# Kernel tuning notes

Hardware: AMD Instinct MI355X
Metric: run time of the kernel (lower is better)

## Reference

```python
import jax, jax.numpy as jnp
import numpy as np

B, S, D, H = 4, 1024, 1024, 16
HD = D // H  # per-head dim = 64
NEG = -10000000000.0


def setup_inputs() -> dict:
    key = jax.random.key(0)
    ks = jax.random.split(key, 12)
    q = jax.random.normal(ks[0], (B, S, D), jnp.float32)
    k = jax.random.normal(ks[1], (B, S, D), jnp.float32)
    v = jax.random.normal(ks[2], (B, S, D), jnp.float32)
    mask = jax.random.randint(ks[3], (B, S, S), 0, 2).astype(jnp.int32)
    sc = 1.0 / np.sqrt(D)
    Wq = jax.random.normal(ks[4], (H, D, HD), jnp.float32) * sc
    bq = jnp.zeros((H, HD), jnp.float32)
    Wk = jax.random.normal(ks[5], (H, D, HD), jnp.float32) * sc
    bk = jnp.zeros((H, HD), jnp.float32)
    Wv = jax.random.normal(ks[6], (H, D, HD), jnp.float32) * sc
    bv = jnp.zeros((H, HD), jnp.float32)
    Wo = jax.random.normal(ks[7], (D, D), jnp.float32) * sc
    bo = jnp.zeros((D,), jnp.float32)
    return {"query": q, "key": k, "value": v, "attention_mask": mask,
            "Wq": Wq, "bq": bq, "Wk": Wk, "bk": bk, "Wv": Wv, "bv": bv,
            "Wo": Wo, "bo": bo}


def reference(query, key, value, attention_mask, Wq, bq, Wk, bk, Wv, bv, Wo, bo):
    # batched per-head projections: [B,S,D] x [H,D,E] -> [B,H,S,E]
    q = jnp.einsum('bsd,hde->bhse', query, Wq) + bq[None, :, None, :]
    k = jnp.einsum('bsd,hde->bhse', key, Wk) + bk[None, :, None, :]
    v = jnp.einsum('bsd,hde->bhse', value, Wv) + bv[None, :, None, :]
    # NOTE: scale uses key_dim (model_size = full D), faithful to source
    score = jnp.einsum('bhse,bhte->bhst', q, k) / jnp.sqrt(jnp.float32(D))
    m = attention_mask.astype(jnp.float32)[:, None, :, :]  # [B,1,S,S]
    score = score + (1.0 - m) * NEG
    attn = jax.nn.softmax(score, axis=-1) * m  # double masking
    heads = jnp.einsum('bhst,bhte->bhse', attn, v)  # [B,H,S,E]
    # concat heads along feature dim (head order preserved)
    heads = heads.transpose(0, 2, 1, 3).reshape(B, S, D)
    return heads @ Wo + bo
```

## Files before the change

kernel.cpp:

```cpp
#include <hip/hip_runtime.h>

#define B_ 4
#define S_ 1024
#define D_ 1024
#define H_ 16
#define E_ 64
#define BS_ (B_*S_)
#define BHSE_ (B_*H_*S_*E_)

typedef __attribute__((ext_vector_type(8))) short bf16x8;
typedef __attribute__((ext_vector_type(4))) float f32x4;
typedef __attribute__((ext_vector_type(4))) unsigned int u32x4;

__device__ __forceinline__ unsigned short f2bf(float f) {
    unsigned int x = __float_as_uint(f);
    x = (x + 0x7FFFu + ((x >> 16) & 1u)) >> 16;
    return (unsigned short)x;
}
__device__ __forceinline__ float bf2f(unsigned short u) {
    return __uint_as_float(((unsigned int)u) << 16);
}
__device__ __forceinline__ float ldin(const void* p, size_t i, int isb) {
    return isb ? bf2f(((const unsigned short*)p)[i]) : ((const float*)p)[i];
}

__device__ __forceinline__ unsigned int cvtpk(float lo, float hi) {
    unsigned int r;
    asm("v_cvt_pk_bf16_f32 %0, %1, %2" : "=v"(r) : "v"(lo), "v"(hi));
    return r;
}
__device__ __forceinline__ unsigned int bperm(int srclane4, unsigned int v) {
    return (unsigned int)__builtin_amdgcn_ds_bpermute(srclane4, (int)v);
}
__device__ __forceinline__ bf16x8 u4bf(u32x4 w) {
    union { u32x4 u; bf16x8 h; } c; c.u = w; return c.h;
}

#if __has_builtin(__builtin_amdgcn_exp2f)
#define EXP2(x) __builtin_amdgcn_exp2f(x)
#else
#define EXP2(x) __expf((x) * 0.6931471805599453f)
#endif

__device__ __forceinline__ void gl2lds16(const void* g, void* l) {
    __builtin_amdgcn_global_load_lds(
        (const __attribute__((address_space(1))) void*)g,
        (__attribute__((address_space(3))) void*)l, 16, 0, 0);
}

__device__ __forceinline__ int detect_isb(const unsigned int* q) {
    unsigned int wv = q[threadIdx.x & 63];
    unsigned int lo = wv & 0xFFFFu;
    unsigned int e = (lo >> 7) & 0xFFu;
    int ok = (lo == 0u) || (e >= 100u && e <= 145u);
    return __popcll(__ballot(ok)) >= 48;
}

__global__ __launch_bounds__(256) void preproc(
        const void* q_, const void* k_, const void* v_, const int* mask,
        const void* Wq, const void* Wk, const void* Wv, const void* Wo,
        const void* bq_, const void* bk_, const void* bv_, const void* bo_,
        unsigned short* WT, float* biases, unsigned long long* packT,
        unsigned short* Aconv) {
    __shared__ unsigned short Tt[64][72];
    const int isb = detect_isb((const unsigned int*)q_);
    const int blk = blockIdx.x, t = threadIdx.x;

    if (blk < 1024) {
        const int c0 = blk & 15, r0 = ((blk >> 4) & 15) * 64, z = blk >> 8;
        const void* src = (z == 0) ? Wq : (z == 1) ? Wk : (z == 2) ? Wv : Wo;
        {
            int dl = t >> 2, qc = t & 3;
            size_t base;
            if (z < 3) base = (size_t)c0 * 65536 + (size_t)(r0 + dl) * 64 + qc * 16;
            else       base = (size_t)(r0 + dl) * 1024 + (size_t)c0 * 64 + qc * 16;
            if (isb) {
                const unsigned short* s = (const unsigned short*)src + base;
                bf16x8 a0 = *(const bf16x8*)s, a1 = *(const bf16x8*)(s + 8);
#pragma unroll
                for (int j = 0; j < 8; j++) {
                    Tt[qc * 16 + j][dl] = (unsigned short)a0[j];
                    Tt[qc * 16 + 8 + j][dl] = (unsigned short)a1[j];
                }
            } else {
                const float* s = (const float*)src + base;
#pragma unroll
                for (int j = 0; j < 16; j++) Tt[qc * 16 + j][dl] = f2bf(s[j]);
            }
        }
        __syncthreads();
        {
            int el = t >> 2, qc = t & 3;
            size_t dst = (size_t)z * D_ * D_ + (size_t)(c0 * 64 + el) * D_ + r0 + qc * 16;
            *(bf16x8*)&WT[dst]     = *(const bf16x8*)&Tt[el][qc * 16];
            *(bf16x8*)&WT[dst + 8] = *(const bf16x8*)&Tt[el][qc * 16 + 8];
        }
        if (z == 3 && ((blk >> 4) & 15) == 0 && c0 < 4) {
            const void* bs = (c0 == 0) ? bq_ : (c0 == 1) ? bk_
                           : (c0 == 2) ? bv_ : bo_;
#pragma unroll
            for (int j = 0; j < 4; j++) {
                int i = t * 4 + j;
                biases[c0 * 1024 + i] = ldin(bs, i, isb);
            }
        }
    } else if (blk < 5120) {
        int unit = (blk - 1024) * 4 + (t >> 6);
        int lane = t & 63;
        int b = unit >> 12, rem = unit & 4095, s0 = (rem >> 4) * 4, kt = rem & 15;
        const int* mb = mask + ((size_t)b * 1024 + s0) * 1024 + kt * 64 + lane;
        unsigned long long bits[4];
#pragma unroll
        for (int j = 0; j < 4; j++) bits[j] = __ballot(mb[j * 1024] != 0);
        if (lane < 4) {
            unsigned long long bb = (lane == 0) ? bits[0] : (lane == 1) ? bits[1]
                                  : (lane == 2) ? bits[2] : bits[3];
            packT[((size_t)b * 16 + kt) * 1024 + s0 + lane] = bb;
        }
    } else {
        if (isb) return;
        int blk2 = blk - 5120;
        const int z = blk2 >> 11;
        const float* s = (z == 0) ? (const float*)q_ : (z == 1) ? (const float*)k_
                                                                : (const float*)v_;
        const size_t i = ((size_t)(blk2 & 2047) * 256 + t) * 8;
        f32x4 a0 = *(const f32x4*)(s + i);
        f32x4 a1 = *(const f32x4*)(s + i + 4);
        bf16x8 o;
#pragma unroll
        for (int j = 0; j < 4; j++) {
            o[j]     = (short)f2bf(a0[j]);
            o[4 + j] = (short)f2bf(a1[j]);
        }
        *(bf16x8*)&Aconv[(size_t)z * ((size_t)BS_ * D_) + i] = o;
    }
}

template<int BM, int BN, int MODE, int MINW>
__global__ __launch_bounds__(256, MINW) void gemm_k(
        const void* A0, const void* A1, const void* A2, const unsigned short* Aconv,
        const unsigned short* BtB, const float* biasB, void* dstB,
        const unsigned int* qdet) {
    constexpr int TOT16 = (BM + BN) * 32;
    constexpr int CALLS = TOT16 / 512;
    constexpr int CPW = CALLS / 4;
    constexpr int MT = BM / 32;
    constexpr int NT = BN / 32;
    __shared__ unsigned short buf[2][TOT16];

    const int fl = detect_isb(qdet);
    const int t = threadIdx.x, lane = t & 63, w = t >> 6;
    const int lm = lane & 15, q4 = lane >> 4;
    const int wm = w >> 1, wn = w & 1;
    const int lr = lane >> 2;
    const int ls = lane & 3;
    const int lg = ls ^ ((lr >> 1) & 3);

    const unsigned short* Abf;
    const unsigned short* Bt;
    const float* bias;
    int z = 0, m0, n0, phase;
    if (MODE == 0) {
        int bid = blockIdx.x + gridDim.x * (blockIdx.y + gridDim.y * blockIdx.z);
        int xcd = bid & 7, idx = bid >> 3;
        z = idx >> 5;
        int r = idx & 31;
        int mt = (xcd << 2) + (r & 3);
        int nt = r >> 2;
        m0 = mt * BM; n0 = nt * BN;
        phase = (nt * 13 + z * 5) & 31;
        const void* Ain = (z == 0) ? A0 : (z == 1 ? A1 : A2);
        Abf = fl ? (const unsigned short*)Ain
                 : Aconv + (size_t)z * ((size_t)BS_ * D_);
        Bt = BtB + (size_t)z * D_ * D_;
        bias = biasB + z * 1024;
    } else {
        Abf = (const unsigned short*)A0;
        Bt = BtB; bias = biasB;
        m0 = blockIdx.x * BM; n0 = blockIdx.y * BN;
        phase = (blockIdx.x * 7 + blockIdx.y * 13) & 31;
    }

    auto stage = [&](int kk, int bi) {
#pragma unroll
        for (int i = 0; i < CPW; ++i) {
            int c = w * CPW + i;
            int row = c * 16 + lr;
            const unsigned short* g;
            if (row < BM)
                g = Abf + (size_t)(m0 + row) * D_ + kk + lg * 8;
            else
                g = Bt + (size_t)(n0 + row - BM) * D_ + kk + lg * 8;
            gl2lds16(g, &buf[bi][c * 512]);
        }
    };

    f32x4 acc[MT][NT];
#pragma unroll
    for (int i = 0; i < MT; i++)
#pragma unroll
        for (int j = 0; j < NT; j++) acc[i][j] = (f32x4){0.f, 0.f, 0.f, 0.f};

    stage((phase & 31) * 32, 0);
    for (int it = 0; it < D_ / 32; ++it) {
        const int bi = it & 1;
        __syncthreads();
        if (it < D_ / 32 - 1) stage(((it + 1 + phase) & 31) * 32, bi ^ 1);

        const unsigned short* As = buf[bi];
        const unsigned short* Bs = buf[bi] + BM * 32;
        bf16x8 af[MT], bv[NT];
#pragma unroll
        for (int mt = 0; mt < MT; mt++) {
            int row = wm * (BM / 2) + mt * 16 + lm;
            af[mt] = *(const bf16x8*)&As[row * 32 + (q4 ^ ((row >> 1) & 3)) * 8];
        }
#pragma unroll
        for (int nt = 0; nt < NT; nt++) {
            int row = wn * (BN / 2) + nt * 16 + lm;
            bv[nt] = *(const bf16x8*)&Bs[row * 32 + (q4 ^ ((row >> 1) & 3)) * 8];
        }
#pragma unroll
        for (int mt = 0; mt < MT; mt++)
#pragma unroll
            for (int nt = 0; nt < NT; nt++)
                acc[mt][nt] = __builtin_amdgcn_mfma_f32_16x16x32_bf16(
                    af[mt], bv[nt], acc[mt][nt], 0, 0, 0);
    }

#pragma unroll
    for (int mt = 0; mt < MT; mt++)
#pragma unroll
        for (int nt = 0; nt < NT; nt++) {
            int N = n0 + wn * (BN / 2) + nt * 16 + lm;
            int Mb = m0 + wm * (BM / 2) + mt * 16 + q4 * 4;
            if (MODE == 0 && z == 2) {
                int bb = Mb >> 10, sb = Mb & 1023, hh = N >> 6, e = N & 63;
                unsigned long long hv = 0;
#pragma unroll
                for (int r = 0; r < 4; r++)
                    hv |= (unsigned long long)f2bf(acc[mt][nt][r] + bias[N]) << (16 * r);
                unsigned short* d16 = (unsigned short*)dstB + (size_t)2 * BHSE_;
                *(unsigned long long*)&d16[(((size_t)(bb * H_ + hh) * E_ + e) << 10) + sb] = hv;
            } else {
#pragma unroll
                for (int r = 0; r < 4; r++) {
                    int M = Mb + r;
                    float v = acc[mt][nt][r] + bias[N];
                    if (MODE == 0) {
                        int bb = M >> 10, s = M & 1023, hh = N >> 6, e = N & 63;
                        unsigned short* d16 = (unsigned short*)dstB + (size_t)z * BHSE_;
                        d16[((size_t)(bb * H_ + hh) * S_ + s) * E_ + e] = f2bf(v);
                    } else {
                        size_t idx = (size_t)M * D_ + N;
                        if (fl) ((unsigned short*)dstB)[idx] = f2bf(v);
                        else    ((float*)dstB)[idx] = v;
                    }
                }
            }
        }
}

__global__ __launch_bounds__(256, 5) void attn64(
        const unsigned short* Qp, const unsigned short* Kp, const unsigned short* VpT,
        const unsigned long long* packT, unsigned short* heads) {
    __shared__ unsigned short KT[2][4096];
    __shared__ unsigned short VT[2][4096];

    const int qt = blockIdx.x, h = blockIdx.y, b = blockIdx.z;
    const int t = threadIdx.x, w = t >> 6, lane = t & 63, lm = lane & 15, q4 = lane >> 4;
    const size_t bh = ((size_t)b * H_ + h) * S_ * E_;
    const unsigned short* Qb = Qp + bh;
    const unsigned short* Kb = Kp + bh;
    const unsigned short* Vb = VpT + bh;
    const int q0 = qt * 64 + w * 16;

    const int l3 = lane >> 3, l7 = lane & 7;
    const int kLaneOff = l3 * 64 + (l7 ^ l3) * 8;
    const int vLaneOff = l3 * 1024 + (l7 ^ l3) * 8;

    const int sw = lm & 7;
    const int c0 = (q4 ^ sw) * 8, c1 = ((q4 ^ 4) ^ sw) * 8;

    const int srcA4 = ((lane & 15) | ((lane & 16) << 1)) << 2;
    const int srcB4 = srcA4 + 64;
    const bool selHi = (lane & 32) != 0;

    bf16x8 bq0 = *(const bf16x8*)&Qb[(size_t)(q0 + lm) * E_ + q4 * 8];
    bf16x8 bq1 = *(const bf16x8*)&Qb[(size_t)(q0 + lm) * E_ + 32 + q4 * 8];

    f32x4 oacc[4];
#pragma unroll
    for (int i = 0; i < 4; i++) oacc[i] = (f32x4){0.f, 0.f, 0.f, 0.f};
    float mrun = -3.0e38f, lrun = 0.f;
    const float scale2 = 0.03125f * 1.4426950408889634f;

#define STAGE(ktile, bufi)                                                    \
    {                                                                         \
        int k0s = (ktile) * 64;                                               \
        _Pragma("unroll")                                                     \
        for (int i_ = 0; i_ < 4; ++i_) {                                      \
            int c_ = w * 4 + i_;                                              \
            if (c_ < 8) {                                                     \
                gl2lds16(Kb + (size_t)k0s * 64 + c_ * 512 + kLaneOff,         \
                         &KT[bufi][c_ * 512]);                                \
            } else {                                                          \
                int cc_ = c_ - 8;                                             \
                gl2lds16(Vb + (size_t)cc_ * 8192 + k0s + vLaneOff,            \
                         &VT[bufi][cc_ * 512]);                               \
            }                                                                 \
        }                                                                     \
    }

    STAGE(0, 0)

    for (int kt = 0; kt < S_ / 64; ++kt) {
        const int bufi = kt & 1;
        __syncthreads();
        if (kt < 15) STAGE(kt + 1, bufi ^ 1)

        unsigned long long mk = packT[((size_t)b * 16 + kt) * 1024 + q0 + lm];

        f32x4 st[4];
#pragma unroll
        for (int jt = 0; jt < 4; ++jt) {
            const unsigned short* kr = &KT[bufi][(jt * 16 + lm) * 64];
            bf16x8 ka0 = *(const bf16x8*)&kr[c0];
            bf16x8 ka1 = *(const bf16x8*)&kr[c1];
            f32x4 zz = (f32x4){0.f, 0.f, 0.f, 0.f};
            zz = __builtin_amdgcn_mfma_f32_16x16x32_bf16(ka0, bq0, zz, 0, 0, 0);
            zz = __builtin_amdgcn_mfma_f32_16x16x32_bf16(ka1, bq1, zz, 0, 0, 0);
            st[jt] = zz;
        }

        float tmx = -3.0e38f;
#pragma unroll
        for (int jt = 0; jt < 4; ++jt)
#pragma unroll
            for (int r = 0; r < 4; r++) tmx = fmaxf(tmx, st[jt][r]);
        tmx = fmaxf(tmx, __shfl_xor(tmx, 16, 64));
        tmx = fmaxf(tmx, __shfl_xor(tmx, 32, 64));
        float pmax = tmx * scale2;

        if (!__all(pmax - mrun <= 8.f)) {
            float mnew = fmaxf(mrun, pmax);
            float alpha = EXP2(mrun - mnew);
            lrun *= alpha;
#pragma unroll
            for (int nt = 0; nt < 4; nt++) oacc[nt] = oacc[nt] * alpha;
            mrun = mnew;
        }
        const float mneg = -mrun;

        unsigned int mn = (unsigned int)(mk >> (q4 * 4));
        unsigned int mh = (unsigned int)(mk >> (q4 * 4 + 32));

        float ssum = 0.f;
        unsigned int cl[8];
#pragma unroll
        for (int jt = 0; jt < 4; ++jt) {
            unsigned int mm = (jt & 2) ? mh : mn;
            const int sh = (jt & 1) * 16;
            float p0 = EXP2(fmaf(st[jt][0], scale2, mneg));
            float p1 = EXP2(fmaf(st[jt][1], scale2, mneg));
            float p2 = EXP2(fmaf(st[jt][2], scale2, mneg));
            float p3 = EXP2(fmaf(st[jt][3], scale2, mneg));
            p0 = (mm & (1u << (sh + 0))) ? p0 : 0.f;
            p1 = (mm & (1u << (sh + 1))) ? p1 : 0.f;
            p2 = (mm & (1u << (sh + 2))) ? p2 : 0.f;
            p3 = (mm & (1u << (sh + 3))) ? p3 : 0.f;
            ssum += (p0 + p1) + (p2 + p3);
            cl[jt * 2]     = cvtpk(p0, p1);
            cl[jt * 2 + 1] = cvtpk(p2, p3);
        }
        ssum += __shfl_xor(ssum, 16, 64);
        ssum += __shfl_xor(ssum, 32, 64);
        lrun += ssum;

        u32x4 w0, w1;
        {
            unsigned int aA0 = bperm(srcA4, cl[0]), aA2 = bperm(srcA4, cl[2]);
            unsigned int aA1 = bperm(srcA4, cl[1]), aA3 = bperm(srcA4, cl[3]);
            unsigned int aB0 = bperm(srcB4, cl[0]), aB2 = bperm(srcB4, cl[2]);
            unsigned int aB1 = bperm(srcB4, cl[1]), aB3 = bperm(srcB4, cl[3]);
            w0 = (u32x4){selHi ? aA2 : aA0, selHi ? aA3 : aA1,
                         selHi ? aB2 : aB0, selHi ? aB3 : aB1};
            unsigned int bA0 = bperm(srcA4, cl[4]), bA2 = bperm(srcA4, cl[6]);
            unsigned int bA1 = bperm(srcA4, cl[5]), bA3 = bperm(srcA4, cl[7]);
            unsigned int bB0 = bperm(srcB4, cl[4]), bB2 = bperm(srcB4, cl[6]);
            unsigned int bB1 = bperm(srcB4, cl[5]), bB3 = bperm(srcB4, cl[7]);
            w1 = (u32x4){selHi ? bA2 : bA0, selHi ? bA3 : bA1,
                         selHi ? bB2 : bB0, selHi ? bB3 : bB1};
        }
        bf16x8 bp0 = u4bf(w0);
        bf16x8 bp1 = u4bf(w1);

#pragma unroll
        for (int nt = 0; nt < 4; nt++) {
            const unsigned short* vr = &VT[bufi][(nt * 16 + lm) * 64];
            bf16x8 va0 = *(const bf16x8*)&vr[c0];
            bf16x8 va1 = *(const bf16x8*)&vr[c1];
            oacc[nt] = __builtin_amdgcn_mfma_f32_16x16x32_bf16(va0, bp0, oacc[nt], 0, 0, 0);
            oacc[nt] = __builtin_amdgcn_mfma_f32_16x16x32_bf16(va1, bp1, oacc[nt], 0, 0, 0);
        }
    }

    float inv = 1.0f / lrun;
#pragma unroll
    for (int nt = 0; nt < 4; nt++) {
        unsigned int lo = cvtpk(oacc[nt][0] * inv, oacc[nt][1] * inv);
        unsigned int hi = cvtpk(oacc[nt][2] * inv, oacc[nt][3] * inv);
        unsigned long long hv = (unsigned long long)lo | ((unsigned long long)hi << 32);
        *(unsigned long long*)&heads[(size_t)(b * S_ + q0 + lm) * D_ + h * E_ + nt * 16 + q4 * 4] = hv;
    }
}

extern "C" void kernel_launch(void* const* d_in, const int* in_sizes, int n_in,
                              void* d_out, int out_size, void* d_ws, size_t ws_size,
                              hipStream_t stream) {
    char* ws = (char*)d_ws;
    unsigned short* WT = (unsigned short*)(ws + 256);
    unsigned short* WqT = WT;
    unsigned short* WoT = WT + (size_t)3 * D_ * D_;
    float* biases = (float*)(WT + (size_t)4 * D_ * D_);
    float* bq = biases;
    float* bo = biases + 3 * 1024;
    unsigned short* Qp = (unsigned short*)(biases + 4 * 1024);
    unsigned short* Kp = Qp + (size_t)BHSE_;
    unsigned short* Vp = Kp + (size_t)BHSE_;
    unsigned short* heads = Vp + (size_t)BHSE_;
    unsigned long long* packT = (unsigned long long*)(heads + (size_t)BHSE_);
    unsigned short* Aconv = (unsigned short*)(packT + (size_t)B_ * 16 * S_);

    preproc<<<11264, 256, 0, stream>>>(
        d_in[0], d_in[1], d_in[2], (const int*)d_in[3],
        d_in[4], d_in[6], d_in[8], d_in[10],
        d_in[5], d_in[7], d_in[9], d_in[11],
        WT, biases, packT, Aconv);
    gemm_k<128, 128, 0, 3><<<dim3(32, 8, 3), 256, 0, stream>>>(
        d_in[0], d_in[1], d_in[2], Aconv, WqT, bq, Qp,
        (const unsigned int*)d_in[0]);
    attn64<<<dim3(16, 16, 4), 256, 0, stream>>>(Qp, Kp, Vp, packT, heads);
    gemm_k<64, 64, 1, 8><<<dim3(64, 16, 1), 256, 0, stream>>>(
        heads, nullptr, nullptr, nullptr, WoT, bo, d_out,
        (const unsigned int*)d_in[0]);
}
```

Measured before the change: 232.4 us.

## Enlarge attention tiles to 128 queries, remap blocks per XCD, prefetch mask

```diff
diff --git a/kernel.cpp b/kernel.cpp
--- a/kernel.cpp
+++ b/kernel.cpp
@@ -177,8 +177,11 @@
     } else {
         Abf = (const unsigned short*)A0;
         Bt = BtB; bias = biasB;
-        m0 = blockIdx.x * BM; n0 = blockIdx.y * BN;
-        phase = (blockIdx.x * 7 + blockIdx.y * 13) & 31;
+        int bid = blockIdx.x + (blockIdx.y << 5);
+        int xcd = bid & 7, idx = bid >> 3;
+        m0 = ((xcd << 2) + (idx & 3)) * BM;
+        n0 = (idx >> 2) * BN;
+        phase = ((idx >> 2) * 13) & 31;
     }
 
     auto stage = [&](int kk, int bi) {
@@ -261,19 +264,24 @@
         }
 }
 
-__global__ __launch_bounds__(256, 5) void attn64(
+__global__ __launch_bounds__(512, 2) void attn64(
         const unsigned short* Qp, const unsigned short* Kp, const unsigned short* VpT,
         const unsigned long long* packT, unsigned short* heads) {
     __shared__ unsigned short KT[2][4096];
     __shared__ unsigned short VT[2][4096];
 
-    const int qt = blockIdx.x, h = blockIdx.y, b = blockIdx.z;
+    const int bid = blockIdx.x + (blockIdx.y << 3) + (blockIdx.z << 7);
+    const int xcd = bid & 7, idx = bid >> 3;
+    const int qt = idx >> 3;
+    const int hb = xcd * 8 + (idx & 7);
+    const int h = hb & 15, b = hb >> 4;
+
     const int t = threadIdx.x, w = t >> 6, lane = t & 63, lm = lane & 15, q4 = lane >> 4;
     const size_t bh = ((size_t)b * H_ + h) * S_ * E_;
     const unsigned short* Qb = Qp + bh;
     const unsigned short* Kb = Kp + bh;
     const unsigned short* Vb = VpT + bh;
-    const int q0 = qt * 64 + w * 16;
+    const int q0 = qt * 128 + w * 16;
 
     const int l3 = lane >> 3, l7 = lane & 7;
     const int kLaneOff = l3 * 64 + (l7 ^ l3) * 8;
@@ -299,8 +307,8 @@
     {                                                                         \
         int k0s = (ktile) * 64;                                               \
         _Pragma("unroll")                                                     \
-        for (int i_ = 0; i_ < 4; ++i_) {                                      \
-            int c_ = w * 4 + i_;                                              \
+        for (int i_ = 0; i_ < 2; ++i_) {                                      \
+            int c_ = w * 2 + i_;                                              \
             if (c_ < 8) {                                                     \
                 gl2lds16(Kb + (size_t)k0s * 64 + c_ * 512 + kLaneOff,         \
                          &KT[bufi][c_ * 512]);                                \
@@ -313,13 +321,16 @@
     }
 
     STAGE(0, 0)
+    unsigned long long mk = packT[(size_t)b * 16 * 1024 + q0 + lm];
 
     for (int kt = 0; kt < S_ / 64; ++kt) {
         const int bufi = kt & 1;
         __syncthreads();
-        if (kt < 15) STAGE(kt + 1, bufi ^ 1)
-
-        unsigned long long mk = packT[((size_t)b * 16 + kt) * 1024 + q0 + lm];
+        unsigned long long mknext = 0;
+        if (kt < 15) {
+            STAGE(kt + 1, bufi ^ 1)
+            mknext = packT[((size_t)b * 16 + kt + 1) * 1024 + q0 + lm];
+        }
 
         f32x4 st[4];
 #pragma unroll
@@ -333,11 +344,11 @@
             st[jt] = zz;
         }
 
-        float tmx = -3.0e38f;
-#pragma unroll
-        for (int jt = 0; jt < 4; ++jt)
-#pragma unroll
-            for (int r = 0; r < 4; r++) tmx = fmaxf(tmx, st[jt][r]);
+        float mx0 = fmaxf(fmaxf(st[0][0], st[0][1]), fmaxf(st[0][2], st[0][3]));
+        float mx1 = fmaxf(fmaxf(st[1][0], st[1][1]), fmaxf(st[1][2], st[1][3]));
+        float mx2 = fmaxf(fmaxf(st[2][0], st[2][1]), fmaxf(st[2][2], st[2][3]));
+        float mx3 = fmaxf(fmaxf(st[3][0], st[3][1]), fmaxf(st[3][2], st[3][3]));
+        float tmx = fmaxf(fmaxf(mx0, mx1), fmaxf(mx2, mx3));
         tmx = fmaxf(tmx, __shfl_xor(tmx, 16, 64));
         tmx = fmaxf(tmx, __shfl_xor(tmx, 32, 64));
         float pmax = tmx * scale2;
@@ -403,6 +414,7 @@
             oacc[nt] = __builtin_amdgcn_mfma_f32_16x16x32_bf16(va0, bp0, oacc[nt], 0, 0, 0);
             oacc[nt] = __builtin_amdgcn_mfma_f32_16x16x32_bf16(va1, bp1, oacc[nt], 0, 0, 0);
         }
+        mk = mknext;
     }
 
     float inv = 1.0f / lrun;
@@ -440,8 +452,8 @@
     gemm_k<128, 128, 0, 3><<<dim3(32, 8, 3), 256, 0, stream>>>(
         d_in[0], d_in[1], d_in[2], Aconv, WqT, bq, Qp,
         (const unsigned int*)d_in[0]);
-    attn64<<<dim3(16, 16, 4), 256, 0, stream>>>(Qp, Kp, Vp, packT, heads);
-    gemm_k<64, 64, 1, 8><<<dim3(64, 16, 1), 256, 0, stream>>>(
+    attn64<<<dim3(8, 16, 4), 512, 0, stream>>>(Qp, Kp, Vp, packT, heads);
+    gemm_k<128, 64, 1, 4><<<dim3(32, 16, 1), 256, 0, stream>>>(
         heads, nullptr, nullptr, nullptr, WoT, bo, d_out,
         (const unsigned int*)d_in[0]);
 }
```

New measurement: 225.8 us. 2.8% less time.
